# Optimization experiments

Hardware: AMD Instinct MI355X
Metric: run time of the kernel (lower is better)

Reference implementation:

```python
import jax, jax.numpy as jnp
import numpy as np

OUT_H = 7
OUT_W = 7
RATIO = 2  # sampling_ratio (static)


def _roi_align(feat, boxes, out_h, out_w, sx, sy, ratio):
    """torchvision-style RoIAlign (aligned=False) on a single image.
    feat: [C,H,W], boxes: [N,4] (x1,y1,x2,y2) in image coords.
    sx, sy: spatial scales (W_feat/W_img, H_feat/H_img). Returns [N,C,out_h,out_w]."""
    C, H, W = feat.shape
    N = boxes.shape[0]
    x1 = boxes[:, 0] * sx
    y1 = boxes[:, 1] * sy
    x2 = boxes[:, 2] * sx
    y2 = boxes[:, 3] * sy
    rw = jnp.maximum(x2 - x1, 1.0)
    rh = jnp.maximum(y2 - y1, 1.0)
    bw = rw / out_w
    bh = rh / out_h
    offs = (jnp.arange(ratio, dtype=feat.dtype) + 0.5) / ratio  # sub-bin sample offsets
    # sample coordinates: [N, out*ratio]
    gy = y1[:, None, None] + (jnp.arange(out_h, dtype=feat.dtype)[None, :, None] + offs[None, None, :]) * bh[:, None, None]
    gx = x1[:, None, None] + (jnp.arange(out_w, dtype=feat.dtype)[None, :, None] + offs[None, None, :]) * bw[:, None, None]
    Y = gy.reshape(N, out_h * ratio)
    X = gx.reshape(N, out_w * ratio)
    vy = (Y >= -1.0) & (Y <= H)
    vx = (X >= -1.0) & (X <= W)
    Yc = jnp.clip(Y, 0.0, H - 1)
    Xc = jnp.clip(X, 0.0, W - 1)
    y0 = jnp.floor(Yc).astype(jnp.int32)
    x0 = jnp.floor(Xc).astype(jnp.int32)
    y1i = jnp.minimum(y0 + 1, H - 1)
    x1i = jnp.minimum(x0 + 1, W - 1)
    ly = Yc - y0.astype(Yc.dtype)
    lx = Xc - x0.astype(Xc.dtype)
    hy = 1.0 - ly
    hx = 1.0 - lx

    def g(yi, xi):  # corner gather -> [C, N, out_h*ratio, out_w*ratio]
        return feat[:, yi[:, :, None], xi[:, None, :]]

    val = (hy[:, :, None] * hx[:, None, :]) * g(y0, x0) \
        + (hy[:, :, None] * lx[:, None, :]) * g(y0, x1i) \
        + (ly[:, :, None] * hx[:, None, :]) * g(y1i, x0) \
        + (ly[:, :, None] * lx[:, None, :]) * g(y1i, x1i)
    valid = vy[:, :, None] & vx[:, None, :]
    val = jnp.where(valid[None], val, 0.0)
    # average over the ratio x ratio sampling grid (always divide by ratio^2)
    val = val.reshape(C, N, out_h, ratio, out_w, ratio).mean(axis=(3, 5))
    return val.transpose(1, 0, 2, 3)


def setup_inputs() -> dict:
    key = jax.random.key(0)
    k0, k1, k2, kb = jax.random.split(key, 4)
    img_h, img_w = 800, 1216
    feat0 = jax.random.normal(k0, (1, 256, 200, 304), dtype=jnp.float32)
    feat1 = jax.random.normal(k1, (1, 256, 100, 152), dtype=jnp.float32)
    feat2 = jax.random.normal(k2, (1, 256, 50, 76), dtype=jnp.float32)
    u = jax.random.uniform(kb, (256, 4), dtype=jnp.float32)
    bx1 = u[:, 0] * (img_w - 32)
    by1 = u[:, 1] * (img_h - 32)
    bw = 16.0 + u[:, 2] * 256.0
    bh = 16.0 + u[:, 3] * 256.0
    bx2 = jnp.minimum(bx1 + bw, float(img_w))
    by2 = jnp.minimum(by1 + bh, float(img_h))
    boxes = jnp.stack([bx1, by1, bx2, by2], axis=1)
    return {"feat0": feat0, "feat1": feat1, "feat2": feat2, "boxes": boxes,
            "img_h": img_h, "img_w": img_w}


def reference(feat0, feat1, feat2, boxes, img_h, img_w):
    _, C, H, W = feat0.shape
    # upsample coarser levels by 2**i, half-pixel bilinear == torch align_corners=False
    ups = [feat0]
    for i, f in enumerate([feat1, feat2], 1):
        s = 2 ** i
        ups.append(jax.image.resize(
            f, (f.shape[0], f.shape[1], f.shape[2] * s, f.shape[3] * s), method='bilinear'))
    fused = jnp.concatenate(ups, axis=1)[0]  # [3C, H, W] (single image)
    sx = W / img_w
    sy = H / img_h
    return _roi_align(fused, boxes, OUT_H, OUT_W, sx, sy, RATIO)
```

## Files before the change

### kernel.cpp

```cpp
#include <hip/hip_runtime.h>
#include <hip/hip_fp16.h>

#define H0 200
#define W0 304
#define H1 100
#define W1 152
#define H2 50
#define W2 76
#define CPL 256
#define CTOT 768
#define OH 7
#define OW 7
#define NPOS 49
#define CBLK 128
#define SROWP 131
#define UXMAX 40

#define P0 (H0*W0)
#define P1 (H1*W1)
#define P2 (H2*W2)
#define T0_OFF ((size_t)0)
#define T1_OFF ((size_t)P0*CPL)
#define T2_OFF ((size_t)P0*CPL + (size_t)P1*CPL)
#define WS_ELEMS ((size_t)P0*CPL + (size_t)P1*CPL + (size_t)P2*CPL)
#define WS_BYTES (WS_ELEMS * 2)

__device__ __forceinline__ float hat01(float d) {
    return fmaxf(0.0f, 1.0f - fabsf(d));
}

__device__ __forceinline__ unsigned short f2h_rne(float x) {
    return __half_as_ushort(__float2half_rn(x));
}

__global__ void __launch_bounds__(256)
transpose_all_kernel(const float* __restrict__ f0, const float* __restrict__ f1,
                     const float* __restrict__ f2,
                     unsigned short* __restrict__ T0,
                     unsigned short* __restrict__ T1,
                     unsigned short* __restrict__ T2, int n0, int n01) {
    __shared__ unsigned short tile[64][72];
    int b = blockIdx.x;
    const float* in; unsigned short* outp; int P; int rel;
    if (b < n0)       { in = f0; outp = T0; P = P0; rel = b; }
    else if (b < n01) { in = f1; outp = T1; P = P1; rel = b - n0; }
    else              { in = f2; outp = T2; P = P2; rel = b - n01; }
    int p0 = (rel >> 2) * 64;
    int c0 = (rel & 3) * 64;

    int q = threadIdx.x & 15;
    int r = threadIdx.x >> 4;
    bool full = (p0 + 64 <= P);
#pragma unroll
    for (int i = 0; i < 4; ++i) {
        int c = c0 + r + 16 * i;
        int p = p0 + 4 * q;
        float4 v;
        if (full) {
            v = *(const float4*)(in + (size_t)c * P + p);
        } else {
            v.x = (p + 0 < P) ? in[(size_t)c * P + p + 0] : 0.0f;
            v.y = (p + 1 < P) ? in[(size_t)c * P + p + 1] : 0.0f;
            v.z = (p + 2 < P) ? in[(size_t)c * P + p + 2] : 0.0f;
            v.w = (p + 3 < P) ? in[(size_t)c * P + p + 3] : 0.0f;
        }
        tile[4 * q + 0][r + 16 * i] = f2h_rne(v.x);
        tile[4 * q + 1][r + 16 * i] = f2h_rne(v.y);
        tile[4 * q + 2][r + 16 * i] = f2h_rne(v.z);
        tile[4 * q + 3][r + 16 * i] = f2h_rne(v.w);
    }
    __syncthreads();
    int q8 = threadIdx.x & 7;
    int r8 = threadIdx.x >> 3;
#pragma unroll
    for (int i = 0; i < 2; ++i) {
        int p = p0 + r8 + 32 * i;
        if (p < P) {
            uint4 w = *(const uint4*)&tile[r8 + 32 * i][8 * q8];
            *(uint4*)(outp + (size_t)p * CPL + c0 + 8 * q8) = w;
        }
    }
}

__device__ __forceinline__ void tap_loop_l0(const unsigned short* __restrict__ T,
                                            const int (*__restrict__ s_idx)[6],
                                            const float (*__restrict__ s_w)[6],
                                            float (*__restrict__ sout)[SROWP],
                                            int pstart, int pcount, int col,
                                            unsigned laneByte) {
    const char* Tb = (const char*)T;
    const __half2 hz = __float2half2_rn(0.0f);
    for (int pi = 0; pi < pcount; ++pi) {
        const int pos = pstart + pi;
        const int oh = pos / 7;
        const int ow = pos - oh * 7;
        unsigned yb[4]; float yw[4];
#pragma unroll
        for (int j2 = 0; j2 < 4; ++j2) {
            yb[j2] = (unsigned)s_idx[oh][j2] + laneByte;
            yw[j2] = s_w[oh][j2];
        }
        unsigned xb[4]; __half2 xw2[4];
#pragma unroll
        for (int j2 = 0; j2 < 4; ++j2) {
            xb[j2] = (unsigned)s_idx[7 + ow][j2];
            xw2[j2] = __float2half2_rn(s_w[7 + ow][j2]);
        }
        float a0 = 0.f, a1 = 0.f, a2 = 0.f, a3 = 0.f;
        float a4 = 0.f, a5 = 0.f, a6 = 0.f, a7 = 0.f;
#pragma unroll
        for (int r = 0; r < 4; ++r) {
            __half2 q0 = hz, q1 = hz, q2 = hz, q3 = hz;
#pragma unroll
            for (int b = 0; b < 4; ++b) {
                uint4 v = *(const uint4*)(Tb + (yb[r] + xb[b]));
                const __half2 xw = xw2[b];
                q0 = __hfma2(xw, *(const __half2*)&v.x, q0);
                q1 = __hfma2(xw, *(const __half2*)&v.y, q1);
                q2 = __hfma2(xw, *(const __half2*)&v.z, q2);
                q3 = __hfma2(xw, *(const __half2*)&v.w, q3);
            }
            const float wa = yw[r];
            a0 = fmaf(wa, __low2float(q0), a0);  a1 = fmaf(wa, __high2float(q0), a1);
            a2 = fmaf(wa, __low2float(q1), a2);  a3 = fmaf(wa, __high2float(q1), a3);
            a4 = fmaf(wa, __low2float(q2), a4);  a5 = fmaf(wa, __high2float(q2), a5);
            a6 = fmaf(wa, __low2float(q3), a6);  a7 = fmaf(wa, __high2float(q3), a7);
        }
        float4 o0, o1;
        o0.x = a0 * 0.25f; o0.y = a1 * 0.25f; o0.z = a2 * 0.25f; o0.w = a3 * 0.25f;
        o1.x = a4 * 0.25f; o1.y = a5 * 0.25f; o1.z = a6 * 0.25f; o1.w = a7 * 0.25f;
        *(float4*)(&sout[pos][col])     = o0;
        *(float4*)(&sout[pos][col + 4]) = o1;
    }
}

template<int TT>
__device__ __forceinline__ void sep_level(const unsigned short* __restrict__ T,
                                          const int (*__restrict__ s_idx)[6],
                                          const float (*__restrict__ s_w)[6],
                                          float (*__restrict__ sout)[SROWP],
                                          float* __restrict__ rowbuf,
                                          int tid, unsigned chalfByte) {
    int xloB = s_idx[7][0], xhiB = xloB;
#pragma unroll
    for (int o = 0; o < 7; ++o) {
#pragma unroll
        for (int t = 0; t < TT; ++t) {
            int v = s_idx[7 + o][t];
            xloB = min(xloB, v);
            xhiB = max(xhiB, v);
        }
    }
    const int ux = ((xhiB - xloB) >> 9) + 1;
    const int g = tid >> 4;
    const int l16 = tid & 15;
    const char* Tbase = (const char*)T + chalfByte + (unsigned)(l16 * 16) + (unsigned)xloB;

    for (int oh = 0; oh < OH; ++oh) {
        for (int s = g; s < ux; s += 16) {
            const char* bp = Tbase + ((unsigned)s << 9);
            float a0 = 0.f, a1 = 0.f, a2 = 0.f, a3 = 0.f;
            float a4 = 0.f, a5 = 0.f, a6 = 0.f, a7 = 0.f;
#pragma unroll
            for (int t = 0; t < TT; ++t) {
                uint4 v = *(const uint4*)(bp + (unsigned)s_idx[oh][t]);
                const float wy = s_w[oh][t];
                float2 f0 = __half22float2(*(const __half2*)&v.x);
                float2 f1 = __half22float2(*(const __half2*)&v.y);
                float2 f2 = __half22float2(*(const __half2*)&v.z);
                float2 f3 = __half22float2(*(const __half2*)&v.w);
                a0 = fmaf(wy, f0.x, a0); a1 = fmaf(wy, f0.y, a1);
                a2 = fmaf(wy, f1.x, a2); a3 = fmaf(wy, f1.y, a3);
                a4 = fmaf(wy, f2.x, a4); a5 = fmaf(wy, f2.y, a5);
                a6 = fmaf(wy, f3.x, a6); a7 = fmaf(wy, f3.y, a7);
            }
            float4* rp = (float4*)&rowbuf[s * CBLK + l16 * 8];
            rp[0] = make_float4(a0, a1, a2, a3);
            rp[1] = make_float4(a4, a5, a6, a7);
        }
        __syncthreads();
        if (tid < 224) {
            const int ow = tid >> 5;
            const int ch = (tid & 31) * 4;
            float b0 = 0.f, b1 = 0.f, b2 = 0.f, b3 = 0.f;
#pragma unroll
            for (int t = 0; t < TT; ++t) {
                int s = (s_idx[7 + ow][t] - xloB) >> 9;
                s = min(s, UXMAX - 1);
                const float wx = s_w[7 + ow][t];
                const float4 rv = *(const float4*)&rowbuf[s * CBLK + ch];
                b0 = fmaf(wx, rv.x, b0); b1 = fmaf(wx, rv.y, b1);
                b2 = fmaf(wx, rv.z, b2); b3 = fmaf(wx, rv.w, b3);
            }
            const int pos = oh * 7 + ow;
            *(float4*)(&sout[pos][ch]) =
                make_float4(b0 * 0.25f, b1 * 0.25f, b2 * 0.25f, b3 * 0.25f);
        }
        __syncthreads();
    }
}

__global__ void __launch_bounds__(256, 3)
roi_align_sep_kernel(const unsigned short* __restrict__ T0p,
                     const unsigned short* __restrict__ T1p,
                     const unsigned short* __restrict__ T2p,
                     const float* __restrict__ boxes,
                     const int* __restrict__ img_h_p,
                     const int* __restrict__ img_w_p,
                     float* __restrict__ out) {
    __shared__ float sout[NPOS][SROWP];
    __shared__ __align__(16) float rowbuf[UXMAX * CBLK];
    __shared__ int   s_idx[14][6];
    __shared__ float s_w[14][6];

    const int n = blockIdx.x;
    const int j = blockIdx.y;
    const int lev = j >> 1;
    const int chalf = j & 1;
    const int tid = threadIdx.x;

    const unsigned short* T; int Hc, Wc; float inv_s;
    if (lev == 0)      { T = T0p; Hc = H0; Wc = W0; inv_s = 1.0f;  }
    else if (lev == 1) { T = T1p; Hc = H1; Wc = W1; inv_s = 0.5f;  }
    else               { T = T2p; Hc = H2; Wc = W2; inv_s = 0.25f; }

    if (tid < 14) {
        int axis = (tid >= 7) ? 1 : 0;
        int o = tid - axis * 7;
        float sx = (float)W0 / (float)img_w_p[0];
        float sy = (float)H0 / (float)img_h_p[0];
        float a1v, bs; int Hf, Hca, mul;
        if (axis) {
            a1v = boxes[n * 4 + 0] * sx;
            float a2v = boxes[n * 4 + 2] * sx;
            bs = fmaxf(a2v - a1v, 1.0f) * (1.0f / (float)OW);
            Hf = W0; Hca = Wc; mul = 1;
        } else {
            a1v = boxes[n * 4 + 1] * sy;
            float a2v = boxes[n * 4 + 3] * sy;
            bs = fmaxf(a2v - a1v, 1.0f) * (1.0f / (float)OH);
            Hf = H0; Hca = Hc; mul = Wc;
        }
        int idx[6]; float w[6];
#pragma unroll
        for (int t = 0; t < 6; ++t) { idx[t] = 0; w[t] = 0.0f; }
        if (lev == 0) {
#pragma unroll
            for (int r2 = 0; r2 < 2; ++r2) {
                float Y = a1v + ((float)o + 0.25f + 0.5f * (float)r2) * bs;
                float v = (Y >= -1.0f && Y <= (float)Hf) ? 1.0f : 0.0f;
                float Yc = fminf(fmaxf(Y, 0.0f), (float)(Hf - 1));
                int y0 = (int)Yc; float lf = Yc - (float)y0;
                idx[2 * r2]     = y0;                  w[2 * r2]     = (1.0f - lf) * v;
                idx[2 * r2 + 1] = min(y0 + 1, Hf - 1); w[2 * r2 + 1] = lf * v;
            }
        } else {
            int bases[2]; float w3[2][3];
#pragma unroll
            for (int r2 = 0; r2 < 2; ++r2) {
                float Y = a1v + ((float)o + 0.25f + 0.5f * (float)r2) * bs;
                float v = (Y >= -1.0f && Y <= (float)Hf) ? 1.0f : 0.0f;
                float Yc = fminf(fmaxf(Y, 0.0f), (float)(Hf - 1));
                int y0 = (int)Yc; float lf = Yc - (float)y0; float hf = 1.0f - lf;
                int yf1 = min(y0 + 1, Hf - 1);
                float yc0 = fminf(fmaxf(((float)y0 + 0.5f) * inv_s - 0.5f, 0.0f), (float)(Hca - 1));
                float yc1 = fminf(fmaxf(((float)yf1 + 0.5f) * inv_s - 0.5f, 0.0f), (float)(Hca - 1));
                int b2 = (int)yc0;
                bases[r2] = b2;
#pragma unroll
                for (int t2 = 0; t2 < 3; ++t2) {
                    float j2 = (float)(b2 + t2);
                    w3[r2][t2] = v * (hf * hat01(yc0 - j2) + lf * hat01(yc1 - j2));
                }
            }
            int dmax = (lev == 1) ? 3 : 2;
            int d = min(max(bases[1] - bases[0], 0), dmax);
            w[0] += w3[0][0]; w[1] += w3[0][1]; w[2] += w3[0][2];
            w[d] += w3[1][0]; w[d + 1] += w3[1][1]; w[d + 2] += w3[1][2];
#pragma unroll
            for (int t = 0; t < 6; ++t) idx[t] = min(bases[0] + t, Hca - 1);
        }
#pragma unroll
        for (int t = 0; t < 6; ++t) { s_idx[tid][t] = idx[t] * mul * CPL * 2; s_w[tid][t] = w[t]; }
    }
    __syncthreads();

    const unsigned chalfByte = (unsigned)(chalf * CBLK) * 2u;

    if (lev == 0) {
        const int grp = tid >> 4;
        const int l16 = tid & 15;
        const int col = l16 * 8;
        const unsigned laneByte = chalfByte + (unsigned)col * 2u;
        const int pstart = 3 * grp;
        const int pcount = (grp == 15) ? 4 : 3;
        tap_loop_l0(T, s_idx, s_w, sout, pstart, pcount, col, laneByte);
    } else if (lev == 1) {
        sep_level<6>(T, s_idx, s_w, sout, rowbuf, tid, chalfByte);
    } else {
        sep_level<5>(T, s_idx, s_w, sout, rowbuf, tid, chalfByte);
    }
    __syncthreads();

    size_t obase = (size_t)n * CTOT * NPOS + (size_t)(lev * CPL + chalf * CBLK) * NPOS;
    int c = tid / NPOS;
    int p = tid - c * NPOS;
    for (int i = tid; i < CBLK * NPOS; i += 256) {
        out[obase + i] = sout[p][c];
        c += 5; p += 11;
        if (p >= NPOS) { p -= NPOS; ++c; }
    }
}

__device__ __forceinline__ void axis_w3_fb(int yf0, int Hf, int Hc, float inv_s,
                                           float lf, int& base, float* w) {
    int yf1 = min(yf0 + 1, Hf - 1);
    float hf = 1.0f - lf;
    float yc0 = fminf(fmaxf(((float)yf0 + 0.5f) * inv_s - 0.5f, 0.0f), (float)(Hc - 1));
    float yc1 = fminf(fmaxf(((float)yf1 + 0.5f) * inv_s - 0.5f, 0.0f), (float)(Hc - 1));
    base = (int)yc0;
#pragma unroll
    for (int r = 0; r < 3; ++r) {
        float j = (float)(base + r);
        w[r] = hf * hat01(yc0 - j) + lf * hat01(yc1 - j);
    }
}

__global__ void __launch_bounds__(256)
roi_align_fused_fb_kernel(const float* __restrict__ f0,
                          const float* __restrict__ f1,
                          const float* __restrict__ f2,
                          const float* __restrict__ boxes,
                          const int* __restrict__ img_h_p,
                          const int* __restrict__ img_w_p,
                          float* __restrict__ out,
                          int total) {
    int i = blockIdx.x * blockDim.x + threadIdx.x;
    if (i >= total) return;
    int ow = i % OW;
    int t = i / OW;
    int oh = t % OH; t /= OH;
    int c = t % CTOT;
    int n = t / CTOT;
    float sx = (float)W0 / (float)img_w_p[0];
    float sy = (float)H0 / (float)img_h_p[0];
    float bx1 = boxes[n * 4 + 0] * sx;
    float by1 = boxes[n * 4 + 1] * sy;
    float bw = fmaxf(boxes[n * 4 + 2] * sx - bx1, 1.0f) / OW;
    float bh = fmaxf(boxes[n * 4 + 3] * sy - by1, 1.0f) / OH;
    int level = c >> 8;
    int cl = c & (CPL - 1);
    const float* f;
    int Hc, Wc; float inv_s;
    if (level == 0)      { f = f0 + (size_t)cl * P0; Hc = H0; Wc = W0; inv_s = 1.0f;  }
    else if (level == 1) { f = f1 + (size_t)cl * P1; Hc = H1; Wc = W1; inv_s = 0.5f;  }
    else                 { f = f2 + (size_t)cl * P2; Hc = H2; Wc = W2; inv_s = 0.25f; }
    float acc = 0.0f;
#pragma unroll
    for (int ry = 0; ry < 2; ++ry) {
        float Y = by1 + ((float)oh + 0.25f + 0.5f * ry) * bh;
        bool vy = (Y >= -1.0f) && (Y <= (float)H0);
        float Yc = fminf(fmaxf(Y, 0.0f), (float)(H0 - 1));
        int y0 = (int)Yc;
        float ly = Yc - (float)y0;
#pragma unroll
        for (int rx = 0; rx < 2; ++rx) {
            float X = bx1 + ((float)ow + 0.25f + 0.5f * rx) * bw;
            bool vx = (X >= -1.0f) && (X <= (float)W0);
            float Xc = fminf(fmaxf(X, 0.0f), (float)(W0 - 1));
            int x0 = (int)Xc;
            float lx = Xc - (float)x0;
            float v;
            if (level == 0) {
                int y1i = min(y0 + 1, H0 - 1), x1i = min(x0 + 1, W0 - 1);
                float hy = 1.0f - ly, hx = 1.0f - lx;
                float v00 = f[y0 * W0 + x0],  v01 = f[y0 * W0 + x1i];
                float v10 = f[y1i * W0 + x0], v11 = f[y1i * W0 + x1i];
                v = hy * (hx * v00 + lx * v01) + ly * (hx * v10 + lx * v11);
            } else {
                int yb, xb; float wy[3], wxl[3];
                axis_w3_fb(y0, H0, Hc, inv_s, ly, yb, wy);
                axis_w3_fb(x0, W0, Wc, inv_s, lx, xb, wxl);
                v = 0.0f;
#pragma unroll
                for (int a = 0; a < 3; ++a) {
                    int row = min(yb + a, Hc - 1) * Wc;
                    float s = 0.0f;
#pragma unroll
                    for (int b = 0; b < 3; ++b)
                        s += wxl[b] * f[row + min(xb + b, Wc - 1)];
                    v += wy[a] * s;
                }
            }
            if (vy && vx) acc += v;
        }
    }
    out[i] = acc * 0.25f;
}

extern "C" void kernel_launch(void* const* d_in, const int* in_sizes, int n_in,
                              void* d_out, int out_size, void* d_ws, size_t ws_size,
                              hipStream_t stream) {
    const float* f0    = (const float*)d_in[0];
    const float* f1    = (const float*)d_in[1];
    const float* f2    = (const float*)d_in[2];
    const float* boxes = (const float*)d_in[3];
    const int* img_h_p = (const int*)d_in[4];
    const int* img_w_p = (const int*)d_in[5];
    float* out = (float*)d_out;
    int N = in_sizes[3] / 4;

    if (ws_size >= WS_BYTES) {
        unsigned short* ws = (unsigned short*)d_ws;
        unsigned short* T0 = ws + T0_OFF;
        unsigned short* T1 = ws + T1_OFF;
        unsigned short* T2 = ws + T2_OFF;
        int n0 = ((P0 + 63) / 64) * 4;
        int n1 = ((P1 + 63) / 64) * 4;
        int n2 = ((P2 + 63) / 64) * 4;
        transpose_all_kernel<<<n0 + n1 + n2, 256, 0, stream>>>(
            f0, f1, f2, T0, T1, T2, n0, n0 + n1);
        roi_align_sep_kernel<<<dim3(N, 6), 256, 0, stream>>>(
            T0, T1, T2, boxes, img_h_p, img_w_p, out);
    } else {
        int total = N * CTOT * OH * OW;
        roi_align_fused_fb_kernel<<<(total + 255) / 256, 256, 0, stream>>>(
            f0, f1, f2, boxes, img_h_p, img_w_p, out, total);
    }
}
```

Before: 165.4 us.

## Replace row-buffer separable pass with per-column streaming over y rows

For the upsampled levels, the two-phase separable filter goes away: it staged horizontally filtered rows in a large shared rowbuf and synchronised per output row. Now each warp owns one output column and streams the contiguous y-row range, doing the x filter in registers and scattering into seven per-row accumulators with the y weights. Boundary taps are folded so repeated clamped rows get merged weights. Dropping rowbuf shrinks shared memory, which allows raising launch bounds to 4 blocks per CU, and the blockIdx-to-level mapping is reordered to schedule level 1 first. The trade-off is that one of eight warps sits idle, and the per-row branchy weight selection adds work.

```diff
diff --git a/kernel.cpp b/kernel.cpp
--- a/kernel.cpp
+++ b/kernel.cpp
@@ -14,7 +14,6 @@
 #define NPOS 49
 #define CBLK 128
 #define SROWP 131
-#define UXMAX 40
 
 #define P0 (H0*W0)
 #define P1 (H1*W1)
@@ -82,6 +81,7 @@
     }
 }
 
+
 __device__ __forceinline__ void tap_loop_l0(const unsigned short* __restrict__ T,
                                             const int (*__restrict__ s_idx)[6],
                                             const float (*__restrict__ s_w)[6],
@@ -113,7 +113,7 @@
             __half2 q0 = hz, q1 = hz, q2 = hz, q3 = hz;
 #pragma unroll
             for (int b = 0; b < 4; ++b) {
-                uint4 v = *(const uint4*)(Tb + (yb[r] + xb[b]));
+                const uint4 v = *(const uint4*)(Tb + (yb[r] + xb[b]));
                 const __half2 xw = xw2[b];
                 q0 = __hfma2(xw, *(const __half2*)&v.x, q0);
                 q1 = __hfma2(xw, *(const __half2*)&v.y, q1);
@@ -134,88 +134,111 @@
     }
 }
 
-template<int TT>
-__device__ __forceinline__ void sep_level(const unsigned short* __restrict__ T,
-                                          const int (*__restrict__ s_idx)[6],
-                                          const float (*__restrict__ s_w)[6],
-                                          float (*__restrict__ sout)[SROWP],
-                                          float* __restrict__ rowbuf,
-                                          int tid, unsigned chalfByte) {
-    int xloB = s_idx[7][0], xhiB = xloB;
+template<int TT, int YSTRIDE>
+__device__ __forceinline__ void sep_cols(const unsigned short* __restrict__ T,
+                                         const int (*__restrict__ s_idx)[6],
+                                         const float (*__restrict__ s_w)[6],
+                                         const int* __restrict__ s_yb,
+                                         float (*__restrict__ sout)[SROWP],
+                                         int tid, unsigned chalfByte, int Hc) {
+    const int g = tid >> 5;
+    const int l = tid & 31;
+    if (g >= 7) return;
+    const int ow = g;
+    unsigned xb[TT]; float xw[TT];
+#pragma unroll
+    for (int t = 0; t < TT; ++t) {
+        xb[t] = (unsigned)s_idx[7 + ow][t] + chalfByte + (unsigned)(l * 8);
+        xw[t] = s_w[7 + ow][t];
+    }
+    int b0[7];
+#pragma unroll
+    for (int o = 0; o < 7; ++o) b0[o] = s_yb[o];
+    int ylo = b0[0], ybmax = b0[0];
+#pragma unroll
+    for (int o = 1; o < 7; ++o) { ylo = min(ylo, b0[o]); ybmax = max(ybmax, b0[o]); }
+    const int yhi = min(ybmax + TT - 1, Hc - 1);
+
+    float acc[7][4];
 #pragma unroll
     for (int o = 0; o < 7; ++o) {
-#pragma unroll
-        for (int t = 0; t < TT; ++t) {
-            int v = s_idx[7 + o][t];
-            xloB = min(xloB, v);
-            xhiB = max(xhiB, v);
-        }
-    }
-    const int ux = ((xhiB - xloB) >> 9) + 1;
-    const int g = tid >> 4;
-    const int l16 = tid & 15;
-    const char* Tbase = (const char*)T + chalfByte + (unsigned)(l16 * 16) + (unsigned)xloB;
-
-    for (int oh = 0; oh < OH; ++oh) {
-        for (int s = g; s < ux; s += 16) {
-            const char* bp = Tbase + ((unsigned)s << 9);
-            float a0 = 0.f, a1 = 0.f, a2 = 0.f, a3 = 0.f;
-            float a4 = 0.f, a5 = 0.f, a6 = 0.f, a7 = 0.f;
-#pragma unroll
-            for (int t = 0; t < TT; ++t) {
-                uint4 v = *(const uint4*)(bp + (unsigned)s_idx[oh][t]);
-                const float wy = s_w[oh][t];
-                float2 f0 = __half22float2(*(const __half2*)&v.x);
-                float2 f1 = __half22float2(*(const __half2*)&v.y);
-                float2 f2 = __half22float2(*(const __half2*)&v.z);
-                float2 f3 = __half22float2(*(const __half2*)&v.w);
-                a0 = fmaf(wy, f0.x, a0); a1 = fmaf(wy, f0.y, a1);
-                a2 = fmaf(wy, f1.x, a2); a3 = fmaf(wy, f1.y, a3);
-                a4 = fmaf(wy, f2.x, a4); a5 = fmaf(wy, f2.y, a5);
-                a6 = fmaf(wy, f3.x, a6); a7 = fmaf(wy, f3.y, a7);
-            }
-            float4* rp = (float4*)&rowbuf[s * CBLK + l16 * 8];
-            rp[0] = make_float4(a0, a1, a2, a3);
-            rp[1] = make_float4(a4, a5, a6, a7);
-        }
-        __syncthreads();
-        if (tid < 224) {
-            const int ow = tid >> 5;
-            const int ch = (tid & 31) * 4;
-            float b0 = 0.f, b1 = 0.f, b2 = 0.f, b3 = 0.f;
-#pragma unroll
-            for (int t = 0; t < TT; ++t) {
-                int s = (s_idx[7 + ow][t] - xloB) >> 9;
-                s = min(s, UXMAX - 1);
-                const float wx = s_w[7 + ow][t];
-                const float4 rv = *(const float4*)&rowbuf[s * CBLK + ch];
-                b0 = fmaf(wx, rv.x, b0); b1 = fmaf(wx, rv.y, b1);
-                b2 = fmaf(wx, rv.z, b2); b3 = fmaf(wx, rv.w, b3);
-            }
-            const int pos = oh * 7 + ow;
-            *(float4*)(&sout[pos][ch]) =
-                make_float4(b0 * 0.25f, b1 * 0.25f, b2 * 0.25f, b3 * 0.25f);
-        }
-        __syncthreads();
-    }
-}
-
-__global__ void __launch_bounds__(256, 3)
-roi_align_sep_kernel(const unsigned short* __restrict__ T0p,
-                     const unsigned short* __restrict__ T1p,
-                     const unsigned short* __restrict__ T2p,
-                     const float* __restrict__ boxes,
-                     const int* __restrict__ img_h_p,
-                     const int* __restrict__ img_w_p,
-                     float* __restrict__ out) {
+        acc[o][0] = 0.f; acc[o][1] = 0.f; acc[o][2] = 0.f; acc[o][3] = 0.f;
+    }
+
+    const char* Tb = (const char*)T;
+
+#define SEP_CONSUME(V, SS)                                                     \
+    {                                                                          \
+        float xr0 = 0.f, xr1 = 0.f, xr2 = 0.f, xr3 = 0.f;                      \
+        _Pragma("unroll")                                                      \
+        for (int t = 0; t < TT; ++t) {                                         \
+            const uint2 vv = V[t];                                             \
+            float2 lo = __half22float2(*(const __half2*)&vv.x);                \
+            float2 hi = __half22float2(*(const __half2*)&vv.y);                \
+            xr0 = fmaf(xw[t], lo.x, xr0); xr1 = fmaf(xw[t], lo.y, xr1);        \
+            xr2 = fmaf(xw[t], hi.x, xr2); xr3 = fmaf(xw[t], hi.y, xr3);        \
+        }                                                                      \
+        _Pragma("unroll")                                                      \
+        for (int o = 0; o < 7; ++o) {                                          \
+            int tt = (SS) - b0[o];                                             \
+            if ((unsigned)tt < (unsigned)TT) {                                 \
+                float wy = s_w[o][tt];                                         \
+                acc[o][0] = fmaf(wy, xr0, acc[o][0]);                          \
+                acc[o][1] = fmaf(wy, xr1, acc[o][1]);                          \
+                acc[o][2] = fmaf(wy, xr2, acc[o][2]);                          \
+                acc[o][3] = fmaf(wy, xr3, acc[o][3]);                          \
+            }                                                                  \
+        }                                                                      \
+    }
+
+    int s = ylo;
+    for (; s + 1 <= yhi; s += 2) {
+        const unsigned sB0 = (unsigned)s * (unsigned)YSTRIDE;
+        uint2 va[TT], vb[TT];
+#pragma unroll
+        for (int t = 0; t < TT; ++t)
+            va[t] = *(const uint2*)(Tb + (sB0 + xb[t]));
+#pragma unroll
+        for (int t = 0; t < TT; ++t)
+            vb[t] = *(const uint2*)(Tb + (sB0 + (unsigned)YSTRIDE + xb[t]));
+        SEP_CONSUME(va, s);
+        SEP_CONSUME(vb, s + 1);
+    }
+    if (s <= yhi) {
+        const unsigned sB0 = (unsigned)s * (unsigned)YSTRIDE;
+        uint2 va[TT];
+#pragma unroll
+        for (int t = 0; t < TT; ++t)
+            va[t] = *(const uint2*)(Tb + (sB0 + xb[t]));
+        SEP_CONSUME(va, s);
+    }
+#undef SEP_CONSUME
+
+    const int ch = l * 4;
+#pragma unroll
+    for (int o = 0; o < 7; ++o) {
+        *(float4*)(&sout[o * 7 + ow][ch]) =
+            make_float4(acc[o][0] * 0.25f, acc[o][1] * 0.25f,
+                        acc[o][2] * 0.25f, acc[o][3] * 0.25f);
+    }
+}
+
+__global__ void __launch_bounds__(256, 4)
+roi_align_sepcol_kernel(const unsigned short* __restrict__ T0p,
+                        const unsigned short* __restrict__ T1p,
+                        const unsigned short* __restrict__ T2p,
+                        const float* __restrict__ boxes,
+                        const int* __restrict__ img_h_p,
+                        const int* __restrict__ img_w_p,
+                        float* __restrict__ out) {
     __shared__ float sout[NPOS][SROWP];
-    __shared__ __align__(16) float rowbuf[UXMAX * CBLK];
     __shared__ int   s_idx[14][6];
     __shared__ float s_w[14][6];
+    __shared__ int   s_yb[7];
 
     const int n = blockIdx.x;
     const int j = blockIdx.y;
-    const int lev = j >> 1;
+    const int lev = (j < 2) ? 1 : ((j < 4) ? 0 : 2);
     const int chalf = j & 1;
     const int tid = threadIdx.x;
 
@@ -279,6 +302,13 @@
             w[d] += w3[1][0]; w[d + 1] += w3[1][1]; w[d + 2] += w3[1][2];
 #pragma unroll
             for (int t = 0; t < 6; ++t) idx[t] = min(bases[0] + t, Hca - 1);
+            if (axis == 0) {
+#pragma unroll
+                for (int t = 4; t >= 0; --t) {
+                    if (bases[0] + t + 1 > Hca - 1) { w[t] += w[t + 1]; w[t + 1] = 0.0f; }
+                }
+                s_yb[o] = bases[0];
+            }
         }
 #pragma unroll
         for (int t = 0; t < 6; ++t) { s_idx[tid][t] = idx[t] * mul * CPL * 2; s_w[tid][t] = w[t]; }
@@ -296,9 +326,9 @@
         const int pcount = (grp == 15) ? 4 : 3;
         tap_loop_l0(T, s_idx, s_w, sout, pstart, pcount, col, laneByte);
     } else if (lev == 1) {
-        sep_level<6>(T, s_idx, s_w, sout, rowbuf, tid, chalfByte);
+        sep_cols<6, W1 * CPL * 2>(T, s_idx, s_w, s_yb, sout, tid, chalfByte, H1);
     } else {
-        sep_level<5>(T, s_idx, s_w, sout, rowbuf, tid, chalfByte);
+        sep_cols<5, W2 * CPL * 2>(T, s_idx, s_w, s_yb, sout, tid, chalfByte, H2);
     }
     __syncthreads();
 
@@ -420,7 +450,7 @@
         int n2 = ((P2 + 63) / 64) * 4;
         transpose_all_kernel<<<n0 + n1 + n2, 256, 0, stream>>>(
             f0, f1, f2, T0, T1, T2, n0, n0 + n1);
-        roi_align_sep_kernel<<<dim3(N, 6), 256, 0, stream>>>(
+        roi_align_sepcol_kernel<<<dim3(N, 6), 256, 0, stream>>>(
             T0, T1, T2, boxes, img_h_p, img_w_p, out);
     } else {
         int total = N * CTOT * OH * OW;
```

Result: faster. 156.6 us (-5.3%).
